# Kernel optimization log

Hardware: AMD Instinct MI355X
Metric: run time of the kernel (lower is better)

## Reference

```python
import jax, jax.numpy as jnp
import numpy as np

EPS = 0.0  # module eps default
N, C = 524288, 128


def setup_inputs() -> dict:
    key = jax.random.key(0)
    x = jax.random.normal(key, (N, C), dtype=jnp.float32)
    return {"x": x}


def reference(x):
    n, c = x.shape
    # mean over batch (H=W=1 in the original NCHW view)
    m = jnp.mean(x, axis=0, keepdims=True)          # [1, C]
    xn = x - m                                      # [N, C]
    # covariance: T @ T.T / (N-1) with T = xn.T -> [C, C]
    f_cov = jnp.einsum('ni,nj->ij', xn, xn) / (n - 1)
    eye = jnp.eye(c, dtype=x.dtype)
    f_cov_shrinked = (1.0 - EPS) * f_cov + EPS * eye
    L = jnp.linalg.cholesky(f_cov_shrinked)         # lower-triangular
    # inv_sqrt = L^{-1} via triangular solve of L @ X = I
    inv_sqrt = jax.scipy.linalg.solve_triangular(L, eye, lower=True)  # [C, C]
    # 1x1 conv with kernel inv_sqrt[o, i] == xn @ inv_sqrt.T
    decorrelated = xn @ inv_sqrt.T                  # [N, C]
    return decorrelated
```

## Files before the change

### kernel.cpp

```cpp
#include <hip/hip_runtime.h>

#define NROWS 524288
#define NCH 128
#define GSTR 40

typedef __attribute__((ext_vector_type(8))) short bf16x8;
typedef __attribute__((ext_vector_type(4))) float f32x4;

#define BARRIER_ND() asm volatile("s_waitcnt lgkmcnt(0)\ns_barrier" ::: "memory")

static __device__ __forceinline__ unsigned short f2bf_rne(float f) {
    unsigned u = __float_as_uint(f);
    return (unsigned short)((u + 0x7FFFu + ((u >> 16) & 1u)) >> 16);
}

static __device__ __forceinline__ bf16x8 ldfrag(const unsigned short* base, int c, int s0) {
    int m = (c >> 3) & 12;
    return *(const bf16x8*)(base + c * GSTR + (((c >> 3) & 1) << 3) + 2 * (s0 ^ m));
}

#define PACKW1(B, c, x0, x1, csacc) do {                                      \
    unsigned u0 = __float_as_uint(x0), u1 = __float_as_uint(x1);              \
    unsigned packH = (u0 >> 16) | (u1 & 0xFFFF0000u);                         \
    float l0_ = 2.0f * ((x0) - __uint_as_float(u0 & 0xFFFF0000u));            \
    float l1_ = 2.0f * ((x1) - __uint_as_float(u1 & 0xFFFF0000u));            \
    unsigned packL = (unsigned)f2bf_rne(l0_) | ((unsigned)f2bf_rne(l1_) << 16); \
    int idx_ = (c) * GSTR + ((cg & 1) << 3) + 2 * (p ^ (cg & 12));            \
    *(unsigned*)&XT[B][0][idx_] = packH;                                      \
    *(unsigned*)&XT[B][1][idx_] = packL;                                      \
    csacc += (x0) + (x1);                                                     \
} while (0)

#define LOADR(ci, r0, r1, r2, r3) do {                                        \
    const float4* s4_ = (const float4*)x + ((size_t)(ci) * 32 + 2 * p) * 32 + cg * 2; \
    r0 = s4_[0]; r1 = s4_[1]; r2 = s4_[32]; r3 = s4_[33];                     \
} while (0)

#define PACKALL(B, r0, r1, r2, r3) do {                                       \
    PACKW1(B, cg * 8 + 0, r0.x, r2.x, cs0);                                   \
    PACKW1(B, cg * 8 + 1, r0.y, r2.y, cs1);                                   \
    PACKW1(B, cg * 8 + 2, r0.z, r2.z, cs2);                                   \
    PACKW1(B, cg * 8 + 3, r0.w, r2.w, cs3);                                   \
    PACKW1(B, cg * 8 + 4, r1.x, r3.x, cs4);                                   \
    PACKW1(B, cg * 8 + 5, r1.y, r3.y, cs5);                                   \
    PACKW1(B, cg * 8 + 6, r1.z, r3.z, cs6);                                   \
    PACKW1(B, cg * 8 + 7, r1.w, r3.w, cs7);                                   \
} while (0)

#define MFMA_STEP(B) do {                                                     \
    const unsigned short* Xh = &XT[B][0][0];                                  \
    const unsigned short* Xl = &XT[B][1][0];                                  \
    bf16x8 ah0 = ldfrag(Xh, (2 * w + 0) * 16 + lc, ls);                       \
    bf16x8 ah1 = ldfrag(Xh, (2 * w + 1) * 16 + lc, ls);                       \
    _Pragma("unroll")                                                         \
    for (int tj = 0; tj < 8; ++tj) {                                          \
        bf16x8 bh = ldfrag(Xh, tj * 16 + lc, ls);                             \
        bf16x8 bl = ldfrag(Xl, tj * 16 + lc, ls);                             \
        acc[0][tj] = __builtin_amdgcn_mfma_f32_16x16x32_bf16(ah0, bh, acc[0][tj], 0, 0, 0); \
        acc[0][tj] = __builtin_amdgcn_mfma_f32_16x16x32_bf16(ah0, bl, acc[0][tj], 0, 0, 0); \
        acc[1][tj] = __builtin_amdgcn_mfma_f32_16x16x32_bf16(ah1, bh, acc[1][tj], 0, 0, 0); \
        acc[1][tj] = __builtin_amdgcn_mfma_f32_16x16x32_bf16(ah1, bl, acc[1][tj], 0, 0, 0); \
    }                                                                         \
} while (0)

template <int STORE>
__global__ __launch_bounds__(256, 4) void k_gram(const float* __restrict__ x,
                                                 float* __restrict__ part,
                                                 float* __restrict__ colpart,
                                                 float* __restrict__ gram,
                                                 float* __restrict__ colsum,
                                                 int cpb) {
    __shared__ __align__(16) unsigned short XT[2][2][128 * GSTR];
    const int tid = threadIdx.x;
    const int w = tid >> 6;
    const int l = tid & 63;
    const int lc = l & 15;
    const int ls = (l >> 4) * 4;
    const int p = tid >> 4;
    const int cg = tid & 15;

    f32x4 acc[2][8];
#pragma unroll
    for (int a = 0; a < 2; ++a)
#pragma unroll
        for (int t = 0; t < 8; ++t) acc[a][t] = (f32x4){0.f, 0.f, 0.f, 0.f};
    float cs0 = 0.f, cs1 = 0.f, cs2 = 0.f, cs3 = 0.f;
    float cs4 = 0.f, cs5 = 0.f, cs6 = 0.f, cs7 = 0.f;

    const int c0 = blockIdx.x * cpb;
    float4 a0, a1, a2, a3, b0, b1, b2, b3;

    LOADR(c0 + 0, a0, a1, a2, a3);
    LOADR(c0 + 1, b0, b1, b2, b3);
    PACKALL(0, a0, a1, a2, a3);
    BARRIER_ND();

#pragma unroll 1
    for (int t = 0; t < cpb; t += 2) {
        MFMA_STEP(0);
        PACKALL(1, b0, b1, b2, b3);
        if (t + 2 < cpb) LOADR(c0 + t + 2, a0, a1, a2, a3);
        BARRIER_ND();
        MFMA_STEP(1);
        if (t + 2 < cpb) {
            PACKALL(0, a0, a1, a2, a3);
            if (t + 3 < cpb) LOADR(c0 + t + 3, b0, b1, b2, b3);
            BARRIER_ND();
        }
    }

    __syncthreads();
    float* cls = (float*)&XT[0][0][0];
    cls[(cg * 8 + 0) * 16 + p] = cs0;
    cls[(cg * 8 + 1) * 16 + p] = cs1;
    cls[(cg * 8 + 2) * 16 + p] = cs2;
    cls[(cg * 8 + 3) * 16 + p] = cs3;
    cls[(cg * 8 + 4) * 16 + p] = cs4;
    cls[(cg * 8 + 5) * 16 + p] = cs5;
    cls[(cg * 8 + 6) * 16 + p] = cs6;
    cls[(cg * 8 + 7) * 16 + p] = cs7;
    __syncthreads();
    float csr = 0.f;
    if (tid < 128) {
#pragma unroll
        for (int pp = 0; pp < 16; ++pp) csr += cls[tid * 16 + pp];
    }

    if (STORE) {
        float* pb = part + (size_t)blockIdx.x * 16384;
#pragma unroll
        for (int a = 0; a < 2; ++a)
#pragma unroll
            for (int tj = 0; tj < 8; ++tj)
#pragma unroll
                for (int q = 0; q < 4; ++q) {
                    int row = (2 * w + a) * 16 + (l >> 4) * 4 + q;
                    int col = tj * 16 + lc;
                    pb[row * NCH + col] = acc[a][tj][q];
                }
        if (tid < 128) colpart[blockIdx.x * 128 + tid] = csr;
    } else {
#pragma unroll
        for (int a = 0; a < 2; ++a)
#pragma unroll
            for (int tj = 0; tj < 8; ++tj)
#pragma unroll
                for (int q = 0; q < 4; ++q) {
                    int row = (2 * w + a) * 16 + (l >> 4) * 4 + q;
                    int col = tj * 16 + lc;
                    atomicAdd(&gram[row * NCH + col], acc[a][tj][q]);
                }
        if (tid < 128) atomicAdd(&colsum[tid], csr);
    }
}

__global__ __launch_bounds__(256) void k_reduce1(const float* __restrict__ part,
                                                 const float* __restrict__ colpart,
                                                 float* __restrict__ part2,
                                                 float* __restrict__ col2,
                                                 int NG) {
    const int b = blockIdx.x;
    if (b < 16 * NG) {
        const int g = b >> 4;
        const int sl = b & 15;
        const int e4 = sl * 1024 + threadIdx.x * 4;
        const float* p0 = part + (size_t)g * 32 * 16384 + e4;
        float4 s = {0.f, 0.f, 0.f, 0.f};
#pragma unroll
        for (int k = 0; k < 32; ++k) {
            float4 v = *(const float4*)(p0 + (size_t)k * 16384);
            s.x += v.x; s.y += v.y; s.z += v.z; s.w += v.w;
        }
        *(float4*)(part2 + (size_t)g * 16384 + e4) = s;
    } else {
        const int g = b - 16 * NG;
        if (threadIdx.x < 128) {
            const float* c0 = colpart + g * 32 * 128 + threadIdx.x;
            float s = 0.f;
#pragma unroll
            for (int k = 0; k < 32; ++k) s += c0[k * 128];
            col2[g * 128 + threadIdx.x] = s;
        }
    }
}

__global__ __launch_bounds__(256) void k_reduce2(const float* __restrict__ part2,
                                                 const float* __restrict__ col2,
                                                 float* __restrict__ gram,
                                                 float* __restrict__ colsum,
                                                 int NG) {
    const int b = blockIdx.x;
    if (b < 16) {
        const int e4 = b * 1024 + threadIdx.x * 4;
        float4 s = {0.f, 0.f, 0.f, 0.f};
#pragma unroll 8
        for (int g = 0; g < NG; ++g) {
            float4 v = *(const float4*)(part2 + (size_t)g * 16384 + e4);
            s.x += v.x; s.y += v.y; s.z += v.z; s.w += v.w;
        }
        *(float4*)(gram + e4) = s;
    } else if (threadIdx.x < 128) {
        float s = 0.f;
#pragma unroll 8
        for (int g = 0; g < NG; ++g) s += col2[g * 128 + threadIdx.x];
        colsum[threadIdx.x] = s;
    }
}

__global__ __launch_bounds__(1024) void k_chol(const float* __restrict__ gram,
                                               const float* __restrict__ colsum,
                                               float* __restrict__ Wout,
                                               float* __restrict__ mout) {
    __shared__ float C[128][264];
    __shared__ __align__(16) float Praw[2][4][264];
    __shared__ float m[128];
    __shared__ float dsq[128];
    const int tid = threadIdx.x;
    const int rs = tid >> 5;
    const int cs = tid & 31;

    if (tid < 128) {
        m[tid] = colsum[tid] * (1.0f / (float)NROWS);
        mout[tid] = m[tid];
    }
    __syncthreads();
    for (int idx = tid; idx < 128 * 128; idx += 1024) {
        int i = idx >> 7, j = idx & 127;
        float g = 0.5f * (gram[i * NCH + j] + gram[j * NCH + i]);
        C[i][128 + j] = (g - (float)NROWS * m[i] * m[j]) * (1.0f / (float)(NROWS - 1));
        C[i][j] = (i == j) ? 1.0f : 0.0f;
    }
    __syncthreads();
    if (tid < 264) {
        int r = tid / 66, g = tid % 66;
        *(float4*)&Praw[0][r][g * 4] = *(const float4*)&C[r][g * 4];
    }
    __syncthreads();

#pragma unroll 1
    for (int kb = 0; kb < 128; kb += 4) {
        const int buf = (kb >> 2) & 1;
        const float* P0 = Praw[buf][0];
        const float* P1 = Praw[buf][1];
        const float* P2 = Praw[buf][2];
        const float* P3 = Praw[buf][3];

        float M00 = P0[128 + kb + 0], M01 = P0[128 + kb + 1], M02 = P0[128 + kb + 2], M03 = P0[128 + kb + 3];
        float M10 = P1[128 + kb + 0], M11 = P1[128 + kb + 1], M12 = P1[128 + kb + 2], M13 = P1[128 + kb + 3];
        float M20 = P2[128 + kb + 0], M21 = P2[128 + kb + 1], M22 = P2[128 + kb + 2], M23 = P2[128 + kb + 3];
        float M30 = P3[128 + kb + 0], M31 = P3[128 + kb + 1], M32 = P3[128 + kb + 2], M33 = P3[128 + kb + 3];

        float rd0 = 1.0f / M00;
        float g10 = M10 * rd0, g20 = M20 * rd0, g30 = M30 * rd0;
        float N11 = M11 - g10 * M01, N12 = M12 - g10 * M02, N13 = M13 - g10 * M03;
        float N21 = M21 - g20 * M01, N22 = M22 - g20 * M02, N23 = M23 - g20 * M03;
        float N31 = M31 - g30 * M01, N32 = M32 - g30 * M02, N33 = M33 - g30 * M03;
        float rd1 = 1.0f / N11;
        float g21 = N21 * rd1, g31 = N31 * rd1;
        float P22 = N22 - g21 * N12, P23 = N23 - g21 * N13;
        float P32 = N32 - g31 * N12, P33 = N33 - g31 * N13;
        float rd2 = 1.0f / P22;
        float g32 = P32 * rd2;
        float Q33 = P33 - g32 * P23;
        float rd3 = 1.0f / Q33;

        float T10 = -g10;
        float T20 = -g20 - g21 * T10, T21 = -g21;
        float T30 = -g30 - g31 * T10 - g32 * T20;
        float T31 = -g31 - g32 * T21;
        float T32 = -g32;

        if (tid == 0) {
            dsq[kb + 0] = 1.0f / sqrtf(M00);
            dsq[kb + 1] = 1.0f / sqrtf(N11);
            dsq[kb + 2] = 1.0f / sqrtf(P22);
            dsq[kb + 3] = 1.0f / sqrtf(Q33);
        }

        const int gs = kb >> 2;
        const bool doB = (cs <= gs);
        const int gRel = gs + 1 + cs;
        const bool doA = (gRel < 32);

        float4 Pb0, Pb1, Pb2, Pb3, Pa0, Pa1, Pa2, Pa3;
        if (doB) {
            Pb0 = *(const float4*)&P0[cs * 4];
            Pb1 = *(const float4*)&P1[cs * 4];
            Pb2 = *(const float4*)&P2[cs * 4];
            Pb3 = *(const float4*)&P3[cs * 4];
        }
        if (doA) {
            Pa0 = *(const float4*)&P0[128 + gRel * 4];
            Pa1 = *(const float4*)&P1[128 + gRel * 4];
            Pa2 = *(const float4*)&P2[128 + gRel * 4];
            Pa3 = *(const float4*)&P3[128 + gRel * 4];
        }

        const int j0 = kb + 1 + rs;
        const int j1 = j0 + 32, j2 = j0 + 64, j3 = j0 + 96;
        const bool v0 = (j0 < 128), v1 = (j1 < 128), v2 = (j2 < 128), v3 = (j3 < 128);
        const int ja0 = v0 ? j0 : 127, ja1 = v1 ? j1 : 127;
        const int ja2 = v2 ? j2 : 127, ja3 = v3 ? j3 : 127;

        float4 q0 = *(const float4*)&C[ja0][128 + kb];
        float4 q1 = *(const float4*)&C[ja1][128 + kb];
        float4 q2 = *(const float4*)&C[ja2][128 + kb];
        float4 q3 = *(const float4*)&C[ja3][128 + kb];

        float c00, c01 = 0.f, c02 = 0.f, c03 = 0.f;
        {
            const int tmax = 1 + rs;
            float f0 = q0.x * rd0;
            c00 = f0;
            if (tmax > 1) {
                float f1 = (q0.y - c00 * M01) * rd1;
                c00 += f1 * T10; c01 = f1;
                if (tmax > 2) {
                    float f2 = (q0.z - c00 * M02 - c01 * M12) * rd2;
                    c00 += f2 * T20; c01 += f2 * T21; c02 = f2;
                    if (tmax > 3) {
                        float f3 = (q0.w - c00 * M03 - c01 * M13 - c02 * M23) * rd3;
                        c00 += f3 * T30; c01 += f3 * T31; c02 += f3 * T32; c03 = f3;
                    }
                }
            }
        }
#define CHAINF(q, d0, d1, d2, d3) \
        float d0, d1, d2, d3; { \
            float f0 = q.x * rd0; d0 = f0; \
            float f1 = (q.y - d0 * M01) * rd1; d0 += f1 * T10; d1 = f1; \
            float f2 = (q.z - d0 * M02 - d1 * M12) * rd2; \
            d0 += f2 * T20; d1 += f2 * T21; d2 = f2; \
            float f3 = (q.w - d0 * M03 - d1 * M13 - d2 * M23) * rd3; \
            d0 += f3 * T30; d1 += f3 * T31; d2 += f3 * T32; d3 = f3; }
        CHAINF(q1, c10, c11, c12, c13)
        CHAINF(q2, c20, c21, c22, c23)
        CHAINF(q3, c30, c31, c32, c33)
#undef CHAINF

#define UPDATE(jv, jj, e0, e1, e2, e3, STG) do {                              \
        if (jv) {                                                             \
            if (doB) {                                                        \
                float4 v = *(const float4*)&C[jj][cs * 4];                    \
                v.x -= e0 * Pb0.x + e1 * Pb1.x + e2 * Pb2.x + e3 * Pb3.x;     \
                v.y -= e0 * Pb0.y + e1 * Pb1.y + e2 * Pb2.y + e3 * Pb3.y;     \
                v.z -= e0 * Pb0.z + e1 * Pb1.z + e2 * Pb2.z + e3 * Pb3.z;     \
                v.w -= e0 * Pb0.w + e1 * Pb1.w + e2 * Pb2.w + e3 * Pb3.w;     \
                *(float4*)&C[jj][cs * 4] = v;                                 \
                if (STG) *(float4*)&Praw[buf ^ 1][jj - kb - 4][cs * 4] = v;   \
            }                                                                 \
            if (doA) {                                                        \
                float4 v = *(const float4*)&C[jj][128 + gRel * 4];            \
                v.x -= e0 * Pa0.x + e1 * Pa1.x + e2 * Pa2.x + e3 * Pa3.x;     \
                v.y -= e0 * Pa0.y + e1 * Pa1.y + e2 * Pa2.y + e3 * Pa3.y;     \
                v.z -= e0 * Pa0.z + e1 * Pa1.z + e2 * Pa2.z + e3 * Pa3.z;     \
                v.w -= e0 * Pa0.w + e1 * Pa1.w + e2 * Pa2.w + e3 * Pa3.w;     \
                *(float4*)&C[jj][128 + gRel * 4] = v;                         \
                if (STG) *(float4*)&Praw[buf ^ 1][jj - kb - 4][128 + gRel * 4] = v; \
            }                                                                 \
        }                                                                     \
} while (0)

        const bool stage0 = v0 && (j0 >= kb + 4) && (j0 < kb + 8);
        UPDATE(v0, j0, c00, c01, c02, c03, stage0);
        UPDATE(v1, j1, c10, c11, c12, c13, false);
        UPDATE(v2, j2, c20, c21, c22, c23, false);
        UPDATE(v3, j3, c30, c31, c32, c33, false);
#undef UPDATE

        if (tid < 4 && kb + 4 < 128) {
            float4 e = {0.f, 0.f, 0.f, 0.f};
            ((float*)&e)[tid] = 1.0f;
            *(float4*)&Praw[buf ^ 1][tid][(gs + 1) * 4] = e;
        }
        __syncthreads();
    }

    for (int idx = tid; idx < 128 * 128; idx += 1024) {
        int j = idx >> 7, c = idx & 127;
        float vv = (c < j) ? C[j][c] * dsq[j] : ((c == j) ? dsq[j] : 0.0f);
        Wout[idx] = vv;
    }
}

__global__ __launch_bounds__(256, 3) void k_apply(const float* __restrict__ x,
                                                  const float* __restrict__ Wg,
                                                  const float* __restrict__ mg,
                                                  float* __restrict__ out) {
    __shared__ __align__(16) unsigned char XS[128 * 256];
    __shared__ float msh[128];
    const int tid = threadIdx.x;
    const int w = tid >> 6, l = tid & 63;
    const int lc = l & 15, la = l >> 4;

    if (tid < 32) *(float4*)&msh[tid * 4] = *(const float4*)&mg[tid * 4];
    __syncthreads();

    bf16x8 wfrag[2][4];
#pragma unroll
    for (int tjl = 0; tjl < 2; ++tjl) {
        int j = (w * 2 + tjl) * 16 + lc;
#pragma unroll
        for (int ks = 0; ks < 4; ++ks) {
            int i0 = ks * 32 + la * 8;
            float4 wa = *(const float4*)&Wg[j * 128 + i0];
            float4 wb = *(const float4*)&Wg[j * 128 + i0 + 4];
            wfrag[tjl][ks][0] = f2bf_rne(wa.x);
            wfrag[tjl][ks][1] = f2bf_rne(wa.y);
            wfrag[tjl][ks][2] = f2bf_rne(wa.z);
            wfrag[tjl][ks][3] = f2bf_rne(wa.w);
            wfrag[tjl][ks][4] = f2bf_rne(wb.x);
            wfrag[tjl][ks][5] = f2bf_rne(wb.y);
            wfrag[tjl][ks][6] = f2bf_rne(wb.z);
            wfrag[tjl][ks][7] = f2bf_rne(wb.w);
        }
    }

    f32x4 acc[8][2];
#pragma unroll
    for (int ti = 0; ti < 8; ++ti)
#pragma unroll
        for (int tjl = 0; tjl < 2; ++tjl) acc[ti][tjl] = (f32x4){0.f, 0.f, 0.f, 0.f};

    const size_t rowbase = (size_t)blockIdx.x * 128;

#pragma unroll
    for (int rep = 0; rep < 16; ++rep) {
        int f = tid + 256 * rep;
        int r = f >> 5, i4 = f & 31;
        float4 vx = *(const float4*)&x[(rowbase + r) * 128 + i4 * 4];
        float4 mv = *(const float4*)&msh[i4 * 4];
        unsigned b0 = f2bf_rne(vx.x - mv.x);
        unsigned b1 = f2bf_rne(vx.y - mv.y);
        unsigned b2 = f2bf_rne(vx.z - mv.z);
        unsigned b3 = f2bf_rne(vx.w - mv.w);
        int g = i4 >> 1, half = i4 & 1;
        unsigned off = r * 256 + ((g ^ (r & 15)) << 4) + half * 8;
        *(uint2*)(XS + off) = make_uint2(b0 | (b1 << 16), b2 | (b3 << 16));
    }
    __syncthreads();

#pragma unroll
    for (int ks = 0; ks < 4; ++ks) {
#pragma unroll
        for (int ti = 0; ti < 8; ++ti) {
            int r = ti * 16 + lc;
            int g = ks * 4 + la;
            bf16x8 af = *(const bf16x8*)(XS + r * 256 + (((g ^ (r & 15))) << 4));
            acc[ti][0] = __builtin_amdgcn_mfma_f32_16x16x32_bf16(af, wfrag[0][ks], acc[ti][0], 0, 0, 0);
            acc[ti][1] = __builtin_amdgcn_mfma_f32_16x16x32_bf16(af, wfrag[1][ks], acc[ti][1], 0, 0, 0);
        }
    }

    float* dst = out + rowbase * 128;
#pragma unroll
    for (int ti = 0; ti < 8; ++ti)
#pragma unroll
        for (int tjl = 0; tjl < 2; ++tjl)
#pragma unroll
            for (int q = 0; q < 4; ++q) {
                int rloc = ti * 16 + la * 4 + q;
                int cglob = (w * 2 + tjl) * 16 + lc;
                dst[rloc * 128 + cglob] = acc[ti][tjl][q];
            }
}

extern "C" void kernel_launch(void* const* d_in, const int* in_sizes, int n_in,
                              void* d_out, int out_size, void* d_ws, size_t ws_size,
                              hipStream_t stream) {
    const float* x = (const float*)d_in[0];
    float* ws = (float*)d_ws;
    float* gram = ws;
    float* colsum = ws + 16384;
    float* W = ws + 16512;
    float* m = ws + 32896;
    float* colpart = ws + 40960;
    float* part = ws + 172032;
    float* out = (float*)d_out;

    int nP = 0;
    for (int cand = 1024; cand >= 256; cand >>= 1) {
        int ng = cand / 32;
        size_t need = ((size_t)172032 + (size_t)cand * 16384 +
                       (size_t)ng * 16384 + (size_t)ng * 128) * sizeof(float);
        if (ws_size >= need) { nP = cand; break; }
    }

    if (nP > 0) {
        const int NG = nP / 32;
        float* part2 = part + (size_t)nP * 16384;
        float* col2 = part2 + (size_t)NG * 16384;
        int cpb = 16384 / nP;
        k_gram<1><<<nP, 256, 0, stream>>>(x, part, colpart, gram, colsum, cpb);
        k_reduce1<<<16 * NG + NG, 256, 0, stream>>>(part, colpart, part2, col2, NG);
        k_reduce2<<<17, 256, 0, stream>>>(part2, col2, gram, colsum, NG);
    } else {
        hipMemsetAsync(d_ws, 0, (16384 + 128) * sizeof(float), stream);
        k_gram<0><<<512, 256, 0, stream>>>(x, part, colpart, gram, colsum, 32);
    }
    k_chol<<<1, 1024, 0, stream>>>(gram, colsum, W, m);
    k_apply<<<NROWS / 128, 256, 0, stream>>>(x, W, m, out);
}
```

Baseline: 275.9 us.

## Overlap bf16 centering/conversion of x with serial Cholesky using extra blocks

The Cholesky kernel now launches 256 blocks: block 0 runs the serial Cholesky while the other blocks centre x, convert it to bf16 in the swizzled LDS layout, and write it to a workspace buffer. The apply kernel then copies the prepared bf16 tile straight into shared memory instead of reading fp32 x and converting it. This hides the conversion work behind the otherwise single-block Cholesky and halves the bytes the apply kernel reads. In exchange it adds a full extra write and read of a 128 MB bf16 buffer and needs a larger workspace.

```diff
diff --git a/kernel.cpp b/kernel.cpp
--- a/kernel.cpp
+++ b/kernel.cpp
@@ -210,7 +210,36 @@
 __global__ __launch_bounds__(1024) void k_chol(const float* __restrict__ gram,
                                                const float* __restrict__ colsum,
                                                float* __restrict__ Wout,
-                                               float* __restrict__ mout) {
+                                               float* __restrict__ mout,
+                                               const float* __restrict__ x,
+                                               unsigned short* __restrict__ xbf) {
+    if (blockIdx.x != 0) {
+        __shared__ float msh[128];
+        if (threadIdx.x < 32) {
+            float4 cv = ((const float4*)colsum)[threadIdx.x];
+            const float sc = 1.0f / (float)NROWS;
+            cv.x *= sc; cv.y *= sc; cv.z *= sc; cv.w *= sc;
+            *(float4*)&msh[threadIdx.x * 4] = cv;
+        }
+        __syncthreads();
+        const size_t stride = (size_t)(gridDim.x - 1) * 1024;
+        const size_t total = (size_t)(NROWS / 128) * 4096;
+        for (size_t f = (size_t)(blockIdx.x - 1) * 1024 + threadIdx.x; f < total; f += stride) {
+            int tile = (int)(f >> 12);
+            int within = (int)(f & 4095);
+            int r = within >> 5, i4 = within & 31;
+            float4 vx = *(const float4*)&x[((size_t)tile * 128 + r) * 128 + i4 * 4];
+            float4 mv = *(const float4*)&msh[i4 * 4];
+            unsigned b0 = f2bf_rne(vx.x - mv.x);
+            unsigned b1 = f2bf_rne(vx.y - mv.y);
+            unsigned b2 = f2bf_rne(vx.z - mv.z);
+            unsigned b3 = f2bf_rne(vx.w - mv.w);
+            size_t d8 = (size_t)tile * 4096 + r * 32 + (((i4 >> 1) ^ (r & 15)) << 1) + (i4 & 1);
+            ((uint2*)xbf)[d8] = make_uint2(b0 | (b1 << 16), b2 | (b3 << 16));
+        }
+        return;
+    }
+
     __shared__ float C[128][264];
     __shared__ __align__(16) float Praw[2][4][264];
     __shared__ float m[128];
@@ -383,7 +412,9 @@
     }
 }
 
+template <int PRE>
 __global__ __launch_bounds__(256, 3) void k_apply(const float* __restrict__ x,
+                                                  const unsigned short* __restrict__ xbf,
                                                   const float* __restrict__ Wg,
                                                   const float* __restrict__ mg,
                                                   float* __restrict__ out) {
@@ -393,8 +424,10 @@
     const int w = tid >> 6, l = tid & 63;
     const int lc = l & 15, la = l >> 4;
 
-    if (tid < 32) *(float4*)&msh[tid * 4] = *(const float4*)&mg[tid * 4];
-    __syncthreads();
+    if (!PRE) {
+        if (tid < 32) *(float4*)&msh[tid * 4] = *(const float4*)&mg[tid * 4];
+        __syncthreads();
+    }
 
     bf16x8 wfrag[2][4];
 #pragma unroll
@@ -424,19 +457,27 @@
 
     const size_t rowbase = (size_t)blockIdx.x * 128;
 
-#pragma unroll
-    for (int rep = 0; rep < 16; ++rep) {
-        int f = tid + 256 * rep;
-        int r = f >> 5, i4 = f & 31;
-        float4 vx = *(const float4*)&x[(rowbase + r) * 128 + i4 * 4];
-        float4 mv = *(const float4*)&msh[i4 * 4];
-        unsigned b0 = f2bf_rne(vx.x - mv.x);
-        unsigned b1 = f2bf_rne(vx.y - mv.y);
-        unsigned b2 = f2bf_rne(vx.z - mv.z);
-        unsigned b3 = f2bf_rne(vx.w - mv.w);
-        int g = i4 >> 1, half = i4 & 1;
-        unsigned off = r * 256 + ((g ^ (r & 15)) << 4) + half * 8;
-        *(uint2*)(XS + off) = make_uint2(b0 | (b1 << 16), b2 | (b3 << 16));
+    if (PRE) {
+        const uint4* src = (const uint4*)(xbf + (size_t)blockIdx.x * 16384);
+        uint4* XS4 = (uint4*)XS;
+#pragma unroll
+        for (int rep = 0; rep < 8; ++rep)
+            XS4[tid + 256 * rep] = src[tid + 256 * rep];
+    } else {
+#pragma unroll
+        for (int rep = 0; rep < 16; ++rep) {
+            int f = tid + 256 * rep;
+            int r = f >> 5, i4 = f & 31;
+            float4 vx = *(const float4*)&x[(rowbase + r) * 128 + i4 * 4];
+            float4 mv = *(const float4*)&msh[i4 * 4];
+            unsigned b0 = f2bf_rne(vx.x - mv.x);
+            unsigned b1 = f2bf_rne(vx.y - mv.y);
+            unsigned b2 = f2bf_rne(vx.z - mv.z);
+            unsigned b3 = f2bf_rne(vx.w - mv.w);
+            int g = i4 >> 1, half = i4 & 1;
+            unsigned off = r * 256 + ((g ^ (r & 15)) << 4) + half * 8;
+            *(uint2*)(XS + off) = make_uint2(b0 | (b1 << 16), b2 | (b3 << 16));
+        }
     }
     __syncthreads();
 
@@ -478,11 +519,12 @@
     float* part = ws + 172032;
     float* out = (float*)d_out;
 
+    const size_t XBF_FLOATS = (size_t)NROWS * NCH / 2;
     int nP = 0;
     for (int cand = 1024; cand >= 256; cand >>= 1) {
         int ng = cand / 32;
         size_t need = ((size_t)172032 + (size_t)cand * 16384 +
-                       (size_t)ng * 16384 + (size_t)ng * 128) * sizeof(float);
+                       (size_t)ng * 16384 + (size_t)ng * 128 + XBF_FLOATS) * sizeof(float);
         if (ws_size >= need) { nP = cand; break; }
     }
 
@@ -490,14 +532,17 @@
         const int NG = nP / 32;
         float* part2 = part + (size_t)nP * 16384;
         float* col2 = part2 + (size_t)NG * 16384;
+        unsigned short* xbf = (unsigned short*)(col2 + (size_t)NG * 128);
         int cpb = 16384 / nP;
         k_gram<1><<<nP, 256, 0, stream>>>(x, part, colpart, gram, colsum, cpb);
         k_reduce1<<<16 * NG + NG, 256, 0, stream>>>(part, colpart, part2, col2, NG);
         k_reduce2<<<17, 256, 0, stream>>>(part2, col2, gram, colsum, NG);
+        k_chol<<<256, 1024, 0, stream>>>(gram, colsum, W, m, x, xbf);
+        k_apply<1><<<NROWS / 128, 256, 0, stream>>>(x, xbf, W, m, out);
     } else {
         hipMemsetAsync(d_ws, 0, (16384 + 128) * sizeof(float), stream);
         k_gram<0><<<512, 256, 0, stream>>>(x, part, colpart, gram, colsum, 32);
-    }
-    k_chol<<<1, 1024, 0, stream>>>(gram, colsum, W, m);
-    k_apply<<<NROWS / 128, 256, 0, stream>>>(x, W, m, out);
-}
+        k_chol<<<1, 1024, 0, stream>>>(gram, colsum, W, m, x, nullptr);
+        k_apply<0><<<NROWS / 128, 256, 0, stream>>>(x, nullptr, W, m, out);
+    }
+}
```

New measurement: 270.2 us (median of 2 runs). 1.02x faster.
